# Kernel optimization log

Hardware: AMD Instinct MI355X
Metric: run time of the kernel (lower is better)

Reference implementation:

```python
import jax, jax.numpy as jnp
import numpy as np

C_S = 1024      # sequence_state_dim
INNER = 32      # inner_dim
C_Z = 128       # pairwise_state_dim
B, L = 1, 1024


def setup_inputs() -> dict:
    key = jax.random.key(0)
    ks = jax.random.split(key, 7)
    inp = {
        "sequence_state": jax.random.normal(ks[0], (B, L, C_S), dtype=jnp.float32),
        "ln_w": jnp.ones((C_S,), dtype=jnp.float32),
        "ln_b": jnp.zeros((C_S,), dtype=jnp.float32),
        # nn.Linear(sequence_state_dim, inner_dim*2): weight [2*INNER, C_S], bias zero-init
        "proj_w": jax.random.normal(ks[1], (2 * INNER, C_S), dtype=jnp.float32) * (1.0 / np.sqrt(C_S)),
        "proj_b": jnp.zeros((2 * INNER,), dtype=jnp.float32),
        # nn.Linear(2*inner_dim, pairwise_state_dim): weight [C_Z, 2*INNER], bias zero-init
        "o_w": jax.random.normal(ks[2], (C_Z, 2 * INNER), dtype=jnp.float32) * (1.0 / np.sqrt(2 * INNER)),
        "o_b": jnp.zeros((C_Z,), dtype=jnp.float32),
    }
    return inp


def reference(sequence_state, ln_w, ln_b, proj_w, proj_b, o_w, o_b):
    # LayerNorm over last dim (eps matches torch default 1e-5)
    mu = jnp.mean(sequence_state, axis=-1, keepdims=True)
    var = jnp.mean(jnp.square(sequence_state - mu), axis=-1, keepdims=True)
    s = (sequence_state - mu) * jax.lax.rsqrt(var + 1e-5) * ln_w + ln_b
    # proj: [B, L, 2*INNER]
    s = jnp.einsum("blc,dc->bld", s, proj_w) + proj_b
    q, k = jnp.split(s, 2, axis=-1)            # each [B, L, INNER]
    # outer product / diff: [B, L, L, INNER] (row index i from k, col index j from q)
    prod = q[:, None, :, :] * k[:, :, None, :]
    diff = q[:, None, :, :] - k[:, :, None, :]
    x = jnp.concatenate([prod, diff], axis=-1)  # [B, L, L, 2*INNER]
    # o_proj -> [B, L, L, C_Z]
    return jnp.einsum("bijd,zd->bijz", x, o_w) + o_b
```

## Files before the change

kernel.cpp:

```cpp
#include <hip/hip_runtime.h>

#define CS   1024
#define CZ   128

typedef __attribute__((ext_vector_type(8))) short short8;
typedef __attribute__((ext_vector_type(4))) float floatx4;

static __device__ __forceinline__ unsigned short f2bf(float f) {
  unsigned int u = __float_as_uint(f);
  u = (u + 0x7fffu + ((u >> 16) & 1u)) >> 16;
  return (unsigned short)u;
}

__global__ __launch_bounds__(256) void prep_kernel(
    const float* __restrict__ seq,
    const float* __restrict__ lnw,
    const float* __restrict__ lnb,
    const float* __restrict__ pw,
    const float* __restrict__ pb,
    unsigned short* __restrict__ q_ws,
    float* __restrict__ k_ws) {
  const int row  = blockIdx.x;
  const int tid  = threadIdx.x;
  const int lane = tid & 63;
  const int wave = tid >> 6;

  __shared__ __align__(16) float snf[CS];
  __shared__ float sred[8];
  __shared__ float pacc[4][64];

  float4 v = *(const float4*)(seq + (size_t)row * CS + tid * 4);
  float s  = v.x + v.y + v.z + v.w;
  float ss = v.x * v.x + v.y * v.y + v.z * v.z + v.w * v.w;
  #pragma unroll
  for (int off = 32; off >= 1; off >>= 1) {
    s  += __shfl_down(s, off, 64);
    ss += __shfl_down(ss, off, 64);
  }
  if (lane == 0) { sred[wave] = s; sred[4 + wave] = ss; }
  __syncthreads();
  const float mu   = (sred[0] + sred[1] + sred[2] + sred[3]) * (1.0f / CS);
  const float var  = (sred[4] + sred[5] + sred[6] + sred[7]) * (1.0f / CS) - mu * mu;
  const float rstd = rsqrtf(var + 1e-5f);
  {
    const int c = tid * 4;
    float4 gw = *(const float4*)(lnw + c);
    float4 gb = *(const float4*)(lnb + c);
    snf[c + 0] = (v.x - mu) * rstd * gw.x + gb.x;
    snf[c + 1] = (v.y - mu) * rstd * gw.y + gb.y;
    snf[c + 2] = (v.z - mu) * rstd * gw.z + gb.z;
    snf[c + 3] = (v.w - mu) * rstd * gw.w + gb.w;
  }
  __syncthreads();

  const int d    = tid & 63;
  const int part = wave;
  const float* pwr = pw + (size_t)d * CS + part * 256;
  const float* snr = snf + part * 256;
  float acc = 0.f;
  #pragma unroll 4
  for (int kk = 0; kk < 32; ++kk) {
    float4 a0 = *(const float4*)(snr + kk * 8);
    float4 a1 = *(const float4*)(snr + kk * 8 + 4);
    float4 b0 = *(const float4*)(pwr + kk * 8);
    float4 b1 = *(const float4*)(pwr + kk * 8 + 4);
    acc += a0.x * b0.x + a0.y * b0.y + a0.z * b0.z + a0.w * b0.w
         + a1.x * b1.x + a1.y * b1.y + a1.z * b1.z + a1.w * b1.w;
  }
  pacc[part][d] = acc;
  __syncthreads();
  if (tid < 64) {
    float r = pacc[0][tid] + pacc[1][tid] + pacc[2][tid] + pacc[3][tid] + pb[tid];
    if (tid < 32) q_ws[row * 32 + tid] = f2bf(r);
    else          k_ws[row * 32 + (tid - 32)] = r;
  }
}

__global__ __launch_bounds__(256, 3) void pair_kernel(
    const unsigned short* __restrict__ q_ws,
    const float* __restrict__ k_ws,
    const float* __restrict__ ow,
    const float* __restrict__ ob,
    float* __restrict__ out) {
  const int bid  = blockIdx.x;
  const int i    = bid >> 2;
  const int jt   = bid & 3;
  const int tid  = threadIdx.x;
  const int lane = tid & 63;
  const int wave = tid >> 6;
  const int quad = lane >> 4;
  const int n16  = lane & 15;

  __shared__ __align__(16) unsigned short Wsh[CZ * 40];
  __shared__ __align__(16) unsigned short Qsh[256 * 40];
  __shared__ float cvec[CZ];

  {
    const int z  = tid >> 1;
    const int dh = (tid & 1) << 4;
    const float* kr  = k_ws + i * 32;
    const float* owr = ow + z * 64;
    #pragma unroll
    for (int t4 = 0; t4 < 4; ++t4) {
      const int d = dh + t4 * 4;
      float4 w1 = *(const float4*)(owr + d);
      float4 w2 = *(const float4*)(owr + 32 + d);
      Wsh[z * 40 + d + 0] = f2bf(kr[d + 0] * w1.x + w2.x);
      Wsh[z * 40 + d + 1] = f2bf(kr[d + 1] * w1.y + w2.y);
      Wsh[z * 40 + d + 2] = f2bf(kr[d + 2] * w1.z + w2.z);
      Wsh[z * 40 + d + 3] = f2bf(kr[d + 3] * w1.w + w2.w);
    }
    if ((tid & 1) == 0) {
      float c = ob[z];
      #pragma unroll
      for (int d = 0; d < 32; ++d) c -= kr[d] * owr[32 + d];
      cvec[z] = c;
    }
  }
  {
    const uint2* qsrc = (const uint2*)(q_ws + (size_t)jt * 256 * 32);
    #pragma unroll
    for (int it = 0; it < 8; ++it) {
      const int n2 = it * 256 + tid;
      const int r  = n2 >> 3, dw = n2 & 7;
      uint2 vv = qsrc[n2];
      *(uint2*)((char*)Qsh + r * 80 + dw * 8) = vv;
    }
  }
  __syncthreads();

  short8 bfr[8];
  float  cv[8];
  #pragma unroll
  for (int c = 0; c < 8; ++c) {
    const int z = c * 16 + n16;
    bfr[c] = *(const short8*)&Wsh[z * 40 + quad * 8];
    cv[c]  = cvec[z];
  }

  const int jbase = jt * 256 + wave * 64;

  #pragma unroll
  for (int js = 0; js < 4; ++js) {
    short8 afr = *(const short8*)&Qsh[(wave * 64 + js * 16 + n16) * 40 + quad * 8];
    float* orow = out + ((size_t)(i * 1024 + jbase + js * 16 + quad * 4)) * CZ + n16;
    #pragma unroll
    for (int c = 0; c < 8; ++c) {
      floatx4 acc = {cv[c], cv[c], cv[c], cv[c]};
      acc = __builtin_amdgcn_mfma_f32_16x16x32_bf16(afr, bfr[c], acc, 0, 0, 0);
      #pragma unroll
      for (int r = 0; r < 4; ++r) {
        orow[r * CZ + c * 16] = acc[r];
      }
    }
  }
}

extern "C" void kernel_launch(void* const* d_in, const int* in_sizes, int n_in,
                              void* d_out, int out_size, void* d_ws, size_t ws_size,
                              hipStream_t stream) {
  const float* seq = (const float*)d_in[0];
  const float* lnw = (const float*)d_in[1];
  const float* lnb = (const float*)d_in[2];
  const float* pw  = (const float*)d_in[3];
  const float* pb  = (const float*)d_in[4];
  const float* ow  = (const float*)d_in[5];
  const float* ob  = (const float*)d_in[6];
  float* out = (float*)d_out;

  unsigned short* q_ws = (unsigned short*)d_ws;
  float*          k_ws = (float*)((char*)d_ws + 64 * 1024);

  prep_kernel<<<1024, 256, 0, stream>>>(seq, lnw, lnb, pw, pb, q_ws, k_ws);
  pair_kernel<<<1024 * 4, 256, 0, stream>>>(q_ws, k_ws, ow, ob, out);
}
```

Baseline: 555.3 us.

## Precompute per-row effective weights in prep kernel and swap MFMA operands for vector stores

The per-row effective weight matrix (k*W1+W2 in bf16) and bias vector are now computed once per row in the prep kernel and written to workspace. Previously the pair kernel rebuilt them in each of its four j-tile blocks. The pair kernel drops shared memory and syncs, loads weight and q fragments straight from global memory, and swaps the MFMA operands so each lane holds four consecutive z outputs, allowing 16-byte vector stores. The cost is an extra 8 MB workspace write and read of precomputed weights. The output store pattern also changes from scattered scalar writes to contiguous float4 writes.

Result: slower. 578.2 us (+4.1%).

```diff
diff --git a/kernel.cpp b/kernel.cpp
--- a/kernel.cpp
+++ b/kernel.cpp
@@ -18,8 +18,11 @@
     const float* __restrict__ lnb,
     const float* __restrict__ pw,
     const float* __restrict__ pb,
+    const float* __restrict__ ow,
+    const float* __restrict__ ob,
     unsigned short* __restrict__ q_ws,
-    float* __restrict__ k_ws) {
+    unsigned short* __restrict__ w_all,
+    float* __restrict__ c_all) {
   const int row  = blockIdx.x;
   const int tid  = threadIdx.x;
   const int lane = tid & 63;
@@ -28,6 +31,7 @@
   __shared__ __align__(16) float snf[CS];
   __shared__ float sred[8];
   __shared__ float pacc[4][64];
+  __shared__ float ksh[32];
 
   float4 v = *(const float4*)(seq + (size_t)row * CS + tid * 4);
   float s  = v.x + v.y + v.z + v.w;
@@ -72,15 +76,44 @@
   if (tid < 64) {
     float r = pacc[0][tid] + pacc[1][tid] + pacc[2][tid] + pacc[3][tid] + pb[tid];
     if (tid < 32) q_ws[row * 32 + tid] = f2bf(r);
-    else          k_ws[row * 32 + (tid - 32)] = r;
+    else          ksh[tid - 32] = r;
+  }
+  __syncthreads();
+
+  const int z  = tid >> 1;
+  const int dh = (tid & 1) << 4;
+  const float* owr = ow + z * 64;
+  unsigned short wloc[16];
+  #pragma unroll
+  for (int t4 = 0; t4 < 4; ++t4) {
+    const int dd = dh + t4 * 4;
+    float4 a = *(const float4*)(owr + dd);
+    float4 b = *(const float4*)(owr + 32 + dd);
+    wloc[t4 * 4 + 0] = f2bf(ksh[dd + 0] * a.x + b.x);
+    wloc[t4 * 4 + 1] = f2bf(ksh[dd + 1] * a.y + b.y);
+    wloc[t4 * 4 + 2] = f2bf(ksh[dd + 2] * a.z + b.z);
+    wloc[t4 * 4 + 3] = f2bf(ksh[dd + 3] * a.w + b.w);
+  }
+  unsigned short* wdst = w_all + (size_t)row * 4096 + tid * 16;
+  *(uint4*)(wdst)     = *(const uint4*)(wloc);
+  *(uint4*)(wdst + 8) = *(const uint4*)(wloc + 8);
+
+  if ((tid & 1) == 0) {
+    float c = ob[z];
+    #pragma unroll
+    for (int t4 = 0; t4 < 8; ++t4) {
+      const int dd = t4 * 4;
+      float4 b = *(const float4*)(owr + 32 + dd);
+      c -= ksh[dd + 0] * b.x + ksh[dd + 1] * b.y + ksh[dd + 2] * b.z + ksh[dd + 3] * b.w;
+    }
+    c_all[row * CZ + z] = c;
   }
 }
 
 __global__ __launch_bounds__(256, 3) void pair_kernel(
     const unsigned short* __restrict__ q_ws,
-    const float* __restrict__ k_ws,
-    const float* __restrict__ ow,
-    const float* __restrict__ ob,
+    const unsigned short* __restrict__ w_all,
+    const float* __restrict__ c_all,
     float* __restrict__ out) {
   const int bid  = blockIdx.x;
   const int i    = bid >> 2;
@@ -91,67 +124,31 @@
   const int quad = lane >> 4;
   const int n16  = lane & 15;
 
-  __shared__ __align__(16) unsigned short Wsh[CZ * 40];
-  __shared__ __align__(16) unsigned short Qsh[256 * 40];
-  __shared__ float cvec[CZ];
+  const unsigned short* wbase = w_all + (size_t)i * 4096 + n16 * 32 + quad * 8;
+  short8 wf[8];
+  #pragma unroll
+  for (int zt = 0; zt < 8; ++zt) wf[zt] = *(const short8*)(wbase + zt * 512);
 
-  {
-    const int z  = tid >> 1;
-    const int dh = (tid & 1) << 4;
-    const float* kr  = k_ws + i * 32;
-    const float* owr = ow + z * 64;
-    #pragma unroll
-    for (int t4 = 0; t4 < 4; ++t4) {
-      const int d = dh + t4 * 4;
-      float4 w1 = *(const float4*)(owr + d);
-      float4 w2 = *(const float4*)(owr + 32 + d);
-      Wsh[z * 40 + d + 0] = f2bf(kr[d + 0] * w1.x + w2.x);
-      Wsh[z * 40 + d + 1] = f2bf(kr[d + 1] * w1.y + w2.y);
-      Wsh[z * 40 + d + 2] = f2bf(kr[d + 2] * w1.z + w2.z);
-      Wsh[z * 40 + d + 3] = f2bf(kr[d + 3] * w1.w + w2.w);
-    }
-    if ((tid & 1) == 0) {
-      float c = ob[z];
-      #pragma unroll
-      for (int d = 0; d < 32; ++d) c -= kr[d] * owr[32 + d];
-      cvec[z] = c;
-    }
-  }
-  {
-    const uint2* qsrc = (const uint2*)(q_ws + (size_t)jt * 256 * 32);
-    #pragma unroll
-    for (int it = 0; it < 8; ++it) {
-      const int n2 = it * 256 + tid;
-      const int r  = n2 >> 3, dw = n2 & 7;
-      uint2 vv = qsrc[n2];
-      *(uint2*)((char*)Qsh + r * 80 + dw * 8) = vv;
-    }
-  }
-  __syncthreads();
-
-  short8 bfr[8];
-  float  cv[8];
+  const float* cbase = c_all + i * CZ + quad * 4;
+  floatx4 cv[8];
   #pragma unroll
-  for (int c = 0; c < 8; ++c) {
-    const int z = c * 16 + n16;
-    bfr[c] = *(const short8*)&Wsh[z * 40 + quad * 8];
-    cv[c]  = cvec[z];
+  for (int zt = 0; zt < 8; ++zt) {
+    float4 t = *(const float4*)(cbase + zt * 16);
+    floatx4 c4; c4[0] = t.x; c4[1] = t.y; c4[2] = t.z; c4[3] = t.w;
+    cv[zt] = c4;
   }
 
   const int jbase = jt * 256 + wave * 64;
-
   #pragma unroll
   for (int js = 0; js < 4; ++js) {
-    short8 afr = *(const short8*)&Qsh[(wave * 64 + js * 16 + n16) * 40 + quad * 8];
-    float* orow = out + ((size_t)(i * 1024 + jbase + js * 16 + quad * 4)) * CZ + n16;
+    const int j = jbase + js * 16 + n16;
+    short8 qf = *(const short8*)(q_ws + j * 32 + quad * 8);
+    float* obase = out + (size_t)(i * 1024 + j) * CZ + quad * 4;
     #pragma unroll
-    for (int c = 0; c < 8; ++c) {
-      floatx4 acc = {cv[c], cv[c], cv[c], cv[c]};
-      acc = __builtin_amdgcn_mfma_f32_16x16x32_bf16(afr, bfr[c], acc, 0, 0, 0);
-      #pragma unroll
-      for (int r = 0; r < 4; ++r) {
-        orow[r * CZ + c * 16] = acc[r];
-      }
+    for (int zt = 0; zt < 8; ++zt) {
+      floatx4 acc = cv[zt];
+      acc = __builtin_amdgcn_mfma_f32_16x16x32_bf16(wf[zt], qf, acc, 0, 0, 0);
+      *(floatx4*)(obase + zt * 16) = acc;
     }
   }
 }
@@ -168,9 +165,10 @@
   const float* ob  = (const float*)d_in[6];
   float* out = (float*)d_out;
 
-  unsigned short* q_ws = (unsigned short*)d_ws;
-  float*          k_ws = (float*)((char*)d_ws + 64 * 1024);
+  unsigned short* q_ws  = (unsigned short*)d_ws;
+  float*          c_all = (float*)((char*)d_ws + 64 * 1024);
+  unsigned short* w_all = (unsigned short*)((char*)d_ws + 640 * 1024);
 
-  prep_kernel<<<1024, 256, 0, stream>>>(seq, lnw, lnb, pw, pb, q_ws, k_ws);
-  pair_kernel<<<1024 * 4, 256, 0, stream>>>(q_ws, k_ws, ow, ob, out);
+  prep_kernel<<<1024, 256, 0, stream>>>(seq, lnw, lnb, pw, pb, ow, ob, q_ws, w_all, c_all);
+  pair_kernel<<<4096, 256, 0, stream>>>(q_ws, w_all, c_all, out);
 }
```
